# Optimization experiments

Hardware: AMD Instinct MI355X
Metric: run time of the kernel (lower is better)

## Reference

```python
import jax, jax.numpy as jnp
import numpy as np

K = 20
EPS = 1e-5

def get_graph_feature(x, k):
    # x: [B, C, N] -> edge features [B, 2C, N, k]
    xt = jnp.swapaxes(x, 1, 2)  # [B, N, C]
    sq = jnp.sum(xt * xt, axis=-1)  # [B, N]
    # negative squared distance: -(|a|^2 + |b|^2 - 2 a.b)
    pair = 2.0 * jnp.einsum('bnc,bmc->bnm', xt, xt) - sq[:, :, None] - sq[:, None, :]
    idx = jax.lax.top_k(pair, k)[1]  # [B, N, k] nearest neighbors (incl. self)
    neigh = jax.vmap(lambda f, i: f[i])(xt, idx)  # [B, N, k, C]
    ctr = xt[:, :, None, :]  # [B, N, 1, C]
    edge = jnp.concatenate([neigh - ctr, jnp.broadcast_to(ctr, neigh.shape)], axis=-1)  # [B,N,k,2C]
    return jnp.transpose(edge, (0, 3, 1, 2))  # [B, 2C, N, k]

def bn_lrelu(y, g, b, axes):
    # training-mode batchnorm (biased batch stats) + LeakyReLU(0.2)
    m = jnp.mean(y, axis=axes, keepdims=True)
    v = jnp.var(y, axis=axes, keepdims=True)
    shape = [1, -1] + [1] * (y.ndim - 2)
    yn = (y - m) / jnp.sqrt(v + EPS) * g.reshape(shape) + b.reshape(shape)
    return jnp.where(yn >= 0, yn, 0.2 * yn)

def edge_block(x, w, g, b, k):
    e = get_graph_feature(x, k)           # [B, 2C, N, k]
    y = jnp.einsum('bcnk,oc->bonk', e, w)  # 1x1 conv2d, no bias
    y = bn_lrelu(y, g, b, (0, 2, 3))
    return jnp.max(y, axis=-1)            # max over k -> [B, O, N]

def setup_inputs() -> dict:
    key = jax.random.key(0)
    ks = jax.random.split(key, 8)
    B, N = 8, 1024
    num_features = 256
    def w(k_, o, i):
        return jax.random.normal(k_, (o, i), dtype=jnp.float32) * (1.0 / np.sqrt(i))
    d = {
        'x': jax.random.normal(ks[0], (B, N, 3), dtype=jnp.float32),
        'w1': w(ks[1], 64, 6),   'g1': jnp.ones(64),  'b1': jnp.zeros(64),
        'w2': w(ks[2], 64, 128), 'g2': jnp.ones(64),  'b2': jnp.zeros(64),
        'w3': w(ks[3], 128, 128),'g3': jnp.ones(128), 'b3': jnp.zeros(128),
        'w4': w(ks[4], 256, 256),'g4': jnp.ones(256), 'b4': jnp.zeros(256),
        'w5': w(ks[5], 512, 512),'g5': jnp.ones(512), 'b5': jnp.zeros(512),
        'wemb': w(ks[6], num_features, 512),
    }
    return d

def reference(x, w1, g1, b1, w2, g2, b2, w3, g3, b3, w4, g4, b4, w5, g5, b5, wemb):
    xc = jnp.swapaxes(x, 2, 1)  # [B, 3, N]
    x1 = edge_block(xc, w1, g1, b1, K)  # [B, 64, N]
    x2 = edge_block(x1, w2, g2, b2, K)  # [B, 64, N]
    x3 = edge_block(x2, w3, g3, b3, K)  # [B, 128, N]
    x4 = edge_block(x3, w4, g4, b4, K)  # [B, 256, N]
    cat = jnp.concatenate([x1, x2, x3, x4], axis=1)  # [B, 512, N]
    y = jnp.einsum('bcn,oc->bon', cat, w5)            # 1x1 conv1d
    y = bn_lrelu(y, g5, b5, (0, 2))
    feat = jnp.max(y, axis=-1)  # [B, 512]
    return feat @ wemb.T        # [B, num_features]
```

## Files before the change

kernel.cpp:

```cpp
#include <hip/hip_runtime.h>
#include <hip/hip_bf16.h>
#include <math.h>

#define BB 8
#define NN 1024
#define KNNK 20
#define LDC 512

typedef __attribute__((ext_vector_type(8))) short bfrag8;
typedef __attribute__((ext_vector_type(4))) float facc4;
typedef __attribute__((ext_vector_type(2))) float v2f;

struct bh8 { __hip_bfloat16 h[8]; };

__device__ __forceinline__ bh8 cvt8(float4 a, float4 b) {
    bh8 v;
    v.h[0] = __float2bfloat16(a.x); v.h[1] = __float2bfloat16(a.y);
    v.h[2] = __float2bfloat16(a.z); v.h[3] = __float2bfloat16(a.w);
    v.h[4] = __float2bfloat16(b.x); v.h[5] = __float2bfloat16(b.y);
    v.h[6] = __float2bfloat16(b.z); v.h[7] = __float2bfloat16(b.w);
    return v;
}

template<int CTRL, int RMASK>
__device__ __forceinline__ float fmax_dpp(float x) {
    int xi = __float_as_int(x);
    int yi = __builtin_amdgcn_update_dpp(xi, xi, CTRL, RMASK, 0xF, false);
    return fmaxf(x, __int_as_float(yi));
}

__device__ __forceinline__ float wave_max64(float x) {
    x = fmax_dpp<0x121, 0xF>(x);
    x = fmax_dpp<0x122, 0xF>(x);
    x = fmax_dpp<0x124, 0xF>(x);
    x = fmax_dpp<0x128, 0xF>(x);
    x = fmax_dpp<0x142, 0xA>(x);
    x = fmax_dpp<0x143, 0xC>(x);
    return __int_as_float(__builtin_amdgcn_readlane(__float_as_int(x), 63));
}

__device__ __forceinline__ void select20_pf(float (*dist)[1024],
                                            int q0, int w, int lane,
                                            int* __restrict__ idxout) {
    float d[2][16];
    int   sl[2][16];
#pragma unroll
    for (int qi = 0; qi < 2; qi++) {
        int row = w * 2 + qi;
#pragma unroll
        for (int j = 0; j < 16; j++) { d[qi][j] = dist[row][lane + 64 * j]; sl[qi][j] = j; }
    }
    constexpr unsigned char CA[63] = {
        0,2,4,6,8,10,12,14,
        0,1,4,5,8,9,12,13,
        1,5,9,13,
        0,1,2,3,8,9,10,11,
        2,3,10,11,
        1,3,5,9,11,13,
        0,1,2,3,4,5,6,7,
        4,5,6,7,
        2,3,6,7,10,11,
        1,3,5,7,9,11,13};
    constexpr unsigned char CB[63] = {
        1,3,5,7,9,11,13,15,
        2,3,6,7,10,11,14,15,
        2,6,10,14,
        4,5,6,7,12,13,14,15,
        4,5,12,13,
        2,4,6,10,12,14,
        8,9,10,11,12,13,14,15,
        8,9,10,11,
        4,5,8,9,12,13,
        2,4,6,8,10,12,14};
#pragma unroll
    for (int c = 0; c < 63; c++) {
        const int a = CA[c], bq = CB[c];
#pragma unroll
        for (int qi = 0; qi < 2; qi++) {
            bool sw = d[qi][a] < d[qi][bq];
            float dmx = sw ? d[qi][bq] : d[qi][a];
            float dmn = sw ? d[qi][a]  : d[qi][bq];
            d[qi][a] = dmx; d[qi][bq] = dmn;
            int smx = sw ? sl[qi][bq] : sl[qi][a];
            int smn = sw ? sl[qi][a]  : sl[qi][bq];
            sl[qi][a] = smx; sl[qi][bq] = smn;
        }
    }
    unsigned long long slp[2];
#pragma unroll
    for (int qi = 0; qi < 2; qi++) {
        int row = w * 2 + qi;
#pragma unroll
        for (int j = 0; j < 16; j++) dist[row][j * 64 + lane] = d[qi][j];
        unsigned long long p = 0;
#pragma unroll
        for (int j = 0; j < 16; j++) p |= (unsigned long long)sl[qi][j] << (4 * j);
        slp[qi] = p;
    }
    float head[2] = {d[0][0], d[1][0]};
    float pf[2]   = {d[0][1], d[1][1]};
    int   ptr[2]  = {2, 2};
    for (int t = 0; t < KNNK; t++) {
#pragma unroll
        for (int qi = 0; qi < 2; qi++) {
            int row = w * 2 + qi;
            float bv = wave_max64(head[qi]);
            unsigned long long ball = __ballot(head[qi] == bv);
            int wl = (int)__builtin_ctzll(ball);
            bool win = (lane == wl);
            if (win) {
                idxout[(q0 + row) * KNNK + t] = (int)(slp[qi] & 15ull) * 64 + lane;
            }
            head[qi] = win ? pf[qi] : head[qi];
            slp[qi]  = win ? (slp[qi] >> 4) : slp[qi];
            if (win) {
                int p = ptr[qi];
                pf[qi] = (p < 16) ? dist[row][p * 64 + lane] : -INFINITY;
                ptr[qi] = p + 1;
            }
        }
    }
}

__device__ __forceinline__ void zero_r1(float* r1s, float* r1q, int O, int tid) {
    for (int i = tid; i < 32 * O; i += 256) { r1s[i] = 0.f; r1q[i] = 0.f; }
}

__global__ __launch_bounds__(256, 4) void knn3_fused(const float* __restrict__ x,
                                                     const float* __restrict__ w1,
                                                     float* __restrict__ zf,
                                                     int* __restrict__ idxout,
                                                     float* __restrict__ r1s, float* __restrict__ r1q) {
    __shared__ float dist[8][1024];
    int tid = threadIdx.x;
    int q0 = (blockIdx.x & 7) * 1024 + (blockIdx.x >> 3) * 8;
    int b = q0 >> 10;
    if (blockIdx.x == 0) zero_r1(r1s, r1q, 64, tid);
    const float* xb = x + (size_t)b * NN * 3;
    int lane = tid & 63, w = tid >> 6;
    float qx[8], qy[8], qz[8];
#pragma unroll
    for (int q = 0; q < 8; q++) {
        const float* qr = xb + (size_t)((q0 & (NN - 1)) + q) * 3;
        qx[q] = qr[0]; qy[q] = qr[1]; qz[q] = qr[2];
    }
#pragma unroll
    for (int cq = 0; cq < 4; cq++) {
        int cand = w * 256 + cq * 64 + lane;
        const float* cr = xb + (size_t)cand * 3;
        float cx = cr[0], cy = cr[1], cz = cr[2];
        float sqc = 0.f;
        sqc += cx * cx; sqc += cy * cy; sqc += cz * cz;
#pragma unroll
        for (int q = 0; q < 8; q++) {
            float d = qx[q] * cx + qy[q] * cy + qz[q] * cz;
            dist[q][cand] = 2.f * d - sqc;
        }
    }
    for (int i = tid; i < 8 * 128; i += 256) {
        int lq = i >> 7, j = i & 127;
        const float* wr = w1 + (j < 64 ? j * 6 : (j - 64) * 6 + 3);
        const float* xr = x + (size_t)(q0 + lq) * 3;
        zf[(size_t)(q0 + lq) * 128 + j] = wr[0] * xr[0] + wr[1] * xr[1] + wr[2] * xr[2];
    }
    __syncthreads();
    select20_pf(dist, q0, w, lane, idxout);
}

template<int C>
__device__ __forceinline__ void knn_body(const float* __restrict__ xT,
                                         const float* __restrict__ sqn,
                                         int* __restrict__ idxout,
                                         float (*dist)[1024], int knnBlk) {
    int tid = threadIdx.x;
    int q0 = (knnBlk & 7) * 1024 + (knnBlk >> 3) * 8;
    int b = q0 >> 10;
    int lane = tid & 63, w = tid >> 6;
    int cand0 = w * 256 + 4 * lane;
    const float* xTb = xT + (size_t)b * C * 1024;
    const float* qrow = xTb + (q0 & (NN - 1));
    float4 sq4 = *(const float4*)(sqn + b * NN + cand0);
    v2f acc2[4][4];
#pragma unroll
    for (int j = 0; j < 4; j++)
#pragma unroll
        for (int p = 0; p < 4; p++) acc2[j][p] = (v2f){0.f, 0.f};
    for (int cg = 0; cg < C / 4; cg++) {
        float4 rch[4];
#pragma unroll
        for (int c = 0; c < 4; c++)
            rch[c] = *(const float4*)(xTb + (size_t)(4 * cg + c) * 1024 + cand0);
#pragma unroll
        for (int c = 0; c < 4; c++) {
            const float* qr = qrow + (size_t)(4 * cg + c) * 1024;
            float4 qa = *(const float4*)qr;
            float4 qb = *(const float4*)(qr + 4);
            v2f qp[4] = {{qa.x, qa.y}, {qa.z, qa.w}, {qb.x, qb.y}, {qb.z, qb.w}};
            float rj[4] = {rch[c].x, rch[c].y, rch[c].z, rch[c].w};
#pragma unroll
            for (int j = 0; j < 4; j++) {
                v2f rr = {rj[j], rj[j]};
                acc2[j][0] += rr * qp[0];
                acc2[j][1] += rr * qp[1];
                acc2[j][2] += rr * qp[2];
                acc2[j][3] += rr * qp[3];
            }
        }
    }
#pragma unroll
    for (int p = 0; p < 4; p++)
#pragma unroll
        for (int half = 0; half < 2; half++) {
            int q = 2 * p + half;
            float4 dv;
            dv.x = 2.f * acc2[0][p][half] - sq4.x;
            dv.y = 2.f * acc2[1][p][half] - sq4.y;
            dv.z = 2.f * acc2[2][p][half] - sq4.z;
            dv.w = 2.f * acc2[3][p][half] - sq4.w;
            *(float4*)&dist[q][cand0] = dv;
        }
    __syncthreads();
    select20_pf(dist, q0, w, lane, idxout);
}

template<int C, int ZO2>
__global__ __launch_bounds__(256, 4) void knnz_fat(const float* __restrict__ xT,
                                                   const float* __restrict__ xt, int off,
                                                   const float* __restrict__ sqn,
                                                   int* __restrict__ idxout,
                                                   const float* __restrict__ w,
                                                   float* __restrict__ zf,
                                                   float* __restrict__ r1s, float* __restrict__ r1q,
                                                   int Onext) {
    __shared__ float dist[8][1024];
    int tid = threadIdx.x;
    if ((int)blockIdx.x < BB * NN / 8) {
        knn_body<C>(xT, sqn, idxout, dist, blockIdx.x);
        return;
    }
    constexpr int ZO = ZO2 / 2;
    int zblk = blockIdx.x - BB * NN / 8;
    if (zblk == 0) zero_r1(r1s, r1q, Onext, tid);
    float (*xs)[C] = (float (*)[C])&dist[0][0];
    int p0 = zblk * 16;
    for (int j = tid; j < 16 * (C / 4); j += 256) {
        int p = j / (C / 4), c4 = j % (C / 4);
        *(float4*)&xs[p][4 * c4] = *(const float4*)(xt + (size_t)(p0 + p) * LDC + off + 4 * c4);
    }
    __syncthreads();
    for (int j = tid; j < ZO2; j += 256) {
        const float* wr = w + (j < ZO ? (size_t)j * 2 * C : (size_t)(j - ZO) * 2 * C + C);
        float acc[16];
#pragma unroll
        for (int p = 0; p < 16; p++) acc[p] = 0.f;
        for (int c4 = 0; c4 < C / 4; c4++) {
            float4 wv = *(const float4*)(wr + 4 * c4);
#pragma unroll
            for (int p = 0; p < 16; p++) {
                float4 xv = *(const float4*)&xs[p][4 * c4];
                acc[p] += wv.x * xv.x + wv.y * xv.y + wv.z * xv.z + wv.w * xv.w;
            }
        }
#pragma unroll
        for (int p = 0; p < 16; p++) zf[(size_t)(p0 + p) * ZO2 + j] = acc[p];
    }
}

__global__ __launch_bounds__(256, 4) void knnz4_fat(const float* __restrict__ xT,
                                                    const float* __restrict__ sqn,
                                                    int* __restrict__ idxout,
                                                    const float* __restrict__ xtcat,
                                                    const float* __restrict__ w4,
                                                    __hip_bfloat16* __restrict__ zf4,
                                                    float* __restrict__ r1s, float* __restrict__ r1q) {
    __shared__ __align__(16) char smem[36864];
    int tid = threadIdx.x;
    if ((int)blockIdx.x < BB * NN / 8) {
        float (*dist)[1024] = (float (*)[1024])smem;
        if (blockIdx.x == 0) zero_r1(r1s, r1q, 256, tid);
        knn_body<128>(xT, sqn, idxout, dist, blockIdx.x);
        return;
    }
    __hip_bfloat16 (*A)[72] = (__hip_bfloat16 (*)[72])smem;
    __hip_bfloat16 (*W)[72] = (__hip_bfloat16 (*)[72])(smem + 18432);
    int zblk = blockIdx.x - BB * NN / 8;
    int mt = zblk >> 2, nt = zblk & 3;
    int lane = tid & 63, wvx = tid >> 6;
    int mw = wvx >> 1, nw = wvx & 1;
    int m0 = lane & 15, qd = lane >> 4;
    int r = tid & 127, hf = tid >> 7;
    facc4 acc[4][4];
    facc4 zz = {0.f, 0.f, 0.f, 0.f};
#pragma unroll
    for (int mi = 0; mi < 4; mi++)
#pragma unroll
        for (int ni = 0; ni < 4; ni++) acc[mi][ni] = zz;
    int j = nt * 128 + r;
    const float* wsrc = w4 + (j < 256 ? (size_t)j * 256 : (size_t)(j - 256) * 256 + 128);
    const float* asrc = xtcat + (size_t)(mt * 128 + r) * 512 + 128;
    for (int kc = 0; kc < 2; kc++) {
#pragma unroll
        for (int u = 0; u < 4; u++) {
            int c0 = kc * 64 + hf * 32 + 8 * u;
            float4 a0 = *(const float4*)(asrc + c0);
            float4 a1 = *(const float4*)(asrc + c0 + 4);
            *(bh8*)&A[r][hf * 32 + 8 * u] = cvt8(a0, a1);
            float4 w0 = *(const float4*)(wsrc + c0);
            float4 w1 = *(const float4*)(wsrc + c0 + 4);
            *(bh8*)&W[r][hf * 32 + 8 * u] = cvt8(w0, w1);
        }
        __syncthreads();
#pragma unroll
        for (int kk = 0; kk < 2; kk++) {
            bfrag8 af[4], bf[4];
#pragma unroll
            for (int mi = 0; mi < 4; mi++)
                af[mi] = *(const bfrag8*)&A[64 * mw + 16 * mi + m0][32 * kk + 8 * qd];
#pragma unroll
            for (int ni = 0; ni < 4; ni++)
                bf[ni] = *(const bfrag8*)&W[64 * nw + 16 * ni + m0][32 * kk + 8 * qd];
#pragma unroll
            for (int mi = 0; mi < 4; mi++)
#pragma unroll
                for (int ni = 0; ni < 4; ni++)
                    acc[mi][ni] = __builtin_amdgcn_mfma_f32_16x16x32_bf16(af[mi], bf[ni], acc[mi][ni], 0, 0, 0);
        }
        __syncthreads();
    }
#pragma unroll
    for (int mi = 0; mi < 4; mi++)
#pragma unroll
        for (int ni = 0; ni < 4; ni++)
#pragma unroll
            for (int rg = 0; rg < 4; rg++) {
                int row = mt * 128 + mw * 64 + mi * 16 + qd * 4 + rg;
                int col = nt * 128 + nw * 64 + ni * 16 + m0;
                zf4[(size_t)row * 512 + col] = __float2bfloat16(acc[mi][ni][rg]);
            }
}

template<int O2>
__global__ __launch_bounds__(256) void gatherstats_k(const float* __restrict__ zf,
                                                     const int* __restrict__ idx,
                                                     float* __restrict__ ymax, float* __restrict__ ymin,
                                                     float* __restrict__ r1s, float* __restrict__ r1q) {
    constexpr int O = O2 / 2;
    __shared__ float red_s[4][O], red_q[4][O];
    int wv = threadIdx.x >> 6, lane = threadIdx.x & 63;
    int n = (blockIdx.x & 7) * 1024 + (blockIdx.x >> 3) * 4 + wv;
    int b = n >> 10;
    const float* zbatch = zf + (size_t)b * NN * O2;
    int nb[KNNK];
#pragma unroll
    for (int k = 0; k < KNNK; k++) nb[k] = idx[n * KNNK + k];
#pragma unroll
    for (int ch = 0; ch < O / 64; ch++) {
        int o = ch * 64 + lane;
        float g[KNNK];
#pragma unroll
        for (int k = 0; k < KNNK; k++) g[k] = zbatch[(size_t)nb[k] * O2 + o];
        float mx = -INFINITY, mn = INFINITY, s = 0.f, ss = 0.f;
#pragma unroll
        for (int k = 0; k < KNNK; k++) {
            float v = g[k];
            mx = fmaxf(mx, v); mn = fminf(mn, v); s += v; ss += v * v;
        }
        float zn  = zf[(size_t)n * O2 + o];
        float zbn = zf[(size_t)n * O2 + O + o];
        float d = zbn - zn;
        mx += d; mn += d;
        ss = ss + 2.f * d * s + (float)KNNK * d * d;
        s  = s + (float)KNNK * d;
        ymax[(size_t)n * O + o] = mx;
        ymin[(size_t)n * O + o] = mn;
        red_s[wv][o] = s;
        red_q[wv][o] = ss;
    }
    __syncthreads();
    int bucket = blockIdx.x & 31;
    for (int o = threadIdx.x; o < O; o += 256) {
        float s4 = red_s[0][o] + red_s[1][o] + red_s[2][o] + red_s[3][o];
        float q4 = red_q[0][o] + red_q[1][o] + red_q[2][o] + red_q[3][o];
        atomicAdd(&r1s[(size_t)bucket * O + o], s4);
        atomicAdd(&r1q[(size_t)bucket * O + o], q4);
    }
}

__global__ __launch_bounds__(256) void gatherstats4_k(const __hip_bfloat16* __restrict__ zf4,
                                                      const int* __restrict__ idx,
                                                      float* __restrict__ ymax, float* __restrict__ ymin,
                                                      float* __restrict__ r1s, float* __restrict__ r1q) {
    __shared__ float red_s[4][256], red_q[4][256];
    int wv = threadIdx.x >> 6, lane = threadIdx.x & 63;
    int n = (blockIdx.x & 7) * 1024 + (blockIdx.x >> 3) * 4 + wv;
    int b = n >> 10;
    const __hip_bfloat16* zbatch = zf4 + (size_t)b * NN * 512;
    int nb[KNNK];
#pragma unroll
    for (int k = 0; k < KNNK; k++) nb[k] = idx[n * KNNK + k];
#pragma unroll
    for (int ch = 0; ch < 4; ch++) {
        int o = ch * 64 + lane;
        float g[KNNK];
#pragma unroll
        for (int k = 0; k < KNNK; k++) g[k] = __bfloat162float(zbatch[(size_t)nb[k] * 512 + o]);
        float mx = -INFINITY, mn = INFINITY, s = 0.f, ss = 0.f;
#pragma unroll
        for (int k = 0; k < KNNK; k++) {
            float v = g[k];
            mx = fmaxf(mx, v); mn = fminf(mn, v); s += v; ss += v * v;
        }
        float zn  = __bfloat162float(zf4[(size_t)n * 512 + o]);
        float zbn = __bfloat162float(zf4[(size_t)n * 512 + 256 + o]);
        float d = zbn - zn;
        mx += d; mn += d;
        ss = ss + 2.f * d * s + (float)KNNK * d * d;
        s  = s + (float)KNNK * d;
        ymax[(size_t)n * 256 + o] = mx;
        ymin[(size_t)n * 256 + o] = mn;
        red_s[wv][o] = s;
        red_q[wv][o] = ss;
    }
    __syncthreads();
    int bucket = blockIdx.x & 31;
    for (int o = threadIdx.x; o < 256; o += 256) {
        float s4 = red_s[0][o] + red_s[1][o] + red_s[2][o] + red_s[3][o];
        float q4 = red_q[0][o] + red_q[1][o] + red_q[2][o] + red_q[3][o];
        atomicAdd(&r1s[(size_t)bucket * 256 + o], s4);
        atomicAdd(&r1q[(size_t)bucket * 256 + o], q4);
    }
}

template<int O>
__global__ __launch_bounds__(256) void epitrans2_k(const float* __restrict__ ymax, const float* __restrict__ ymin,
                                                   const float* __restrict__ r1s, const float* __restrict__ r1q,
                                                   const float* __restrict__ g, const float* __restrict__ beta,
                                                   double invM,
                                                   float* __restrict__ xtcat, int off_out,
                                                   float* __restrict__ xT, float* __restrict__ sqn,
                                                   __hip_bfloat16* __restrict__ xbf) {
    __shared__ float tile[64][O + 1];
    __shared__ float ssh[O], tth[O];
    int n0 = blockIdx.x * 64;
    int b = n0 >> 10;
    int tid = threadIdx.x;
    for (int o = tid; o < O; o += 256) {
        double sd = 0.0, qd = 0.0;
        for (int r = 0; r < 32; r++) { sd += r1s[(size_t)r * O + o]; qd += r1q[(size_t)r * O + o]; }
        double mean = sd * invM;
        double var = qd * invM - mean * mean;
        float inv = (float)(1.0 / sqrt(var + 1e-5));
        float sc = g[o] * inv;
        ssh[o] = sc;
        tth[o] = beta[o] - (float)mean * sc;
    }
    __syncthreads();
    for (int i = tid; i < 64 * O; i += 256) {
        int nl = i / O;
        int o = i & (O - 1);
        int n = n0 + nl;
        float sc = ssh[o];
        float v = sc >= 0.f ? ymax[(size_t)n * O + o] : ymin[(size_t)n * O + o];
        float y = sc * v + tth[o];
        y = y >= 0.f ? y : 0.2f * y;
        xtcat[(size_t)n * LDC + off_out + o] = y;
        xbf[(size_t)n * LDC + off_out + o] = __float2bfloat16(y);
        tile[nl][o] = y;
    }
    __syncthreads();
    if (tid < 64) {
        float sq = 0.f;
        for (int c = 0; c < O; c++) { float v = tile[tid][c]; sq += v * v; }
        sqn[n0 + tid] = sq;
    }
    int r = tid >> 4, cq = tid & 15;
#pragma unroll
    for (int ct = 0; ct < O / 16; ct++) {
        int c = ct * 16 + r;
        float4 ov;
        ov.x = tile[4 * cq + 0][c];
        ov.y = tile[4 * cq + 1][c];
        ov.z = tile[4 * cq + 2][c];
        ov.w = tile[4 * cq + 3][c];
        *(float4*)(xT + ((size_t)b * O + c) * 1024 + (n0 & (NN - 1)) + 4 * cq) = ov;
    }
}

__global__ __launch_bounds__(256) void epilogue4_k(const float* __restrict__ ymax, const float* __restrict__ ymin,
                                                   const float* __restrict__ r1s, const float* __restrict__ r1q,
                                                   const float* __restrict__ g, const float* __restrict__ beta,
                                                   double invM,
                                                   __hip_bfloat16* __restrict__ xbf) {
    __shared__ float ssh[256], tth[256];
    int n0 = blockIdx.x * 64;
    int tid = threadIdx.x;
    {
        int o = tid;
        double sd = 0.0, qd = 0.0;
        for (int r = 0; r < 32; r++) { sd += r1s[(size_t)r * 256 + o]; qd += r1q[(size_t)r * 256 + o]; }
        double mean = sd * invM;
        double var = qd * invM - mean * mean;
        float inv = (float)(1.0 / sqrt(var + 1e-5));
        float sc = g[o] * inv;
        ssh[o] = sc;
        tth[o] = beta[o] - (float)mean * sc;
    }
    __syncthreads();
    for (int i = tid; i < 64 * 256; i += 256) {
        int nl = i >> 8;
        int o = i & 255;
        int n = n0 + nl;
        float sc = ssh[o];
        float v = sc >= 0.f ? ymax[(size_t)n * 256 + o] : ymin[(size_t)n * 256 + o];
        float y = sc * v + tth[o];
        y = y >= 0.f ? y : 0.2f * y;
        xbf[(size_t)n * LDC + 256 + o] = __float2bfloat16(y);
    }
}

__global__ __launch_bounds__(256) void gemm5_mfma(const __hip_bfloat16* __restrict__ xbf,
                                                  const float* __restrict__ w5,
                                                  float* __restrict__ pmax, float* __restrict__ pmn,
                                                  float* __restrict__ ps, float* __restrict__ pq) {
    __shared__ __hip_bfloat16 A[128][72];
    __shared__ __hip_bfloat16 W[128][72];
    int mt = blockIdx.x >> 2, nt = blockIdx.x & 3;
    int tid = threadIdx.x;
    int lane = tid & 63, wvx = tid >> 6;
    int mw = wvx >> 1, nw = wvx & 1;
    int m0 = lane & 15, qd = lane >> 4;
    int r = tid & 127, hf = tid >> 7;
    facc4 acc[4][4];
    facc4 zz = {0.f, 0.f, 0.f, 0.f};
#pragma unroll
    for (int mi = 0; mi < 4; mi++)
#pragma unroll
        for (int ni = 0; ni < 4; ni++) acc[mi][ni] = zz;
    for (int kc = 0; kc < 8; kc++) {
        const __hip_bfloat16* ap = xbf + (size_t)(mt * 128 + r) * 512 + kc * 64 + hf * 32;
        const float* wp = w5 + (size_t)(nt * 128 + r) * 512 + kc * 64 + hf * 32;
#pragma unroll
        for (int u = 0; u < 4; u++) {
            bh8 av = *(const bh8*)(ap + 8 * u);
            *(bh8*)&A[r][hf * 32 + 8 * u] = av;
            float4 w0 = *(const float4*)(wp + 8 * u);
            float4 w1 = *(const float4*)(wp + 8 * u + 4);
            *(bh8*)&W[r][hf * 32 + 8 * u] = cvt8(w0, w1);
        }
        __syncthreads();
#pragma unroll
        for (int kk = 0; kk < 2; kk++) {
            bfrag8 af[4], bf[4];
#pragma unroll
            for (int mi = 0; mi < 4; mi++)
                af[mi] = *(const bfrag8*)&A[64 * mw + 16 * mi + m0][32 * kk + 8 * qd];
#pragma unroll
            for (int ni = 0; ni < 4; ni++)
                bf[ni] = *(const bfrag8*)&W[64 * nw + 16 * ni + m0][32 * kk + 8 * qd];
#pragma unroll
            for (int mi = 0; mi < 4; mi++)
#pragma unroll
                for (int ni = 0; ni < 4; ni++)
                    acc[mi][ni] = __builtin_amdgcn_mfma_f32_16x16x32_bf16(af[mi], bf[ni], acc[mi][ni], 0, 0, 0);
        }
        __syncthreads();
    }
#pragma unroll
    for (int mi = 0; mi < 4; mi++) {
        int grp = mt * 8 + mw * 4 + mi;
#pragma unroll
        for (int ni = 0; ni < 4; ni++) {
            float mx = -INFINITY, mn = INFINITY, s = 0.f, ss = 0.f;
#pragma unroll
            for (int rg = 0; rg < 4; rg++) {
                float v = acc[mi][ni][rg];
                mx = fmaxf(mx, v); mn = fminf(mn, v); s += v; ss += v * v;
            }
#pragma unroll
            for (int m = 16; m < 64; m <<= 1) {
                mx = fmaxf(mx, __shfl_xor(mx, m));
                mn = fminf(mn, __shfl_xor(mn, m));
                s += __shfl_xor(s, m);
                ss += __shfl_xor(ss, m);
            }
            if (qd == 0) {
                int o = nt * 128 + nw * 64 + ni * 16 + m0;
                pmax[(size_t)grp * 512 + o] = mx;
                pmn [(size_t)grp * 512 + o] = mn;
                ps  [(size_t)grp * 512 + o] = s;
                pq  [(size_t)grp * 512 + o] = ss;
            }
        }
    }
}

__global__ __launch_bounds__(256) void bnstat5_k(const float* __restrict__ ps, const float* __restrict__ pq,
                                                 const float* __restrict__ g, const float* __restrict__ beta,
                                                 float* __restrict__ s_out, float* __restrict__ t_out) {
    __shared__ double lds_s[4][8], lds_q[4][8];
    int tid = threadIdx.x;
    int lane = tid & 63, wv = tid >> 6;
    int ol = lane & 7;
    int rg = wv * 8 + (lane >> 3);
    int o = blockIdx.x * 8 + ol;
    double s = 0.0, q = 0.0;
    for (int r = rg; r < 512; r += 32) {
        s += ps[(size_t)r * 512 + o];
        q += pq[(size_t)r * 512 + o];
    }
    s += __shfl_xor(s, 8);  q += __shfl_xor(q, 8);
    s += __shfl_xor(s, 16); q += __shfl_xor(q, 16);
    s += __shfl_xor(s, 32); q += __shfl_xor(q, 32);
    if (lane < 8) { lds_s[wv][ol] = s; lds_q[wv][ol] = q; }
    __syncthreads();
    if (tid < 8) {
        s = lds_s[0][tid] + lds_s[1][tid] + lds_s[2][tid] + lds_s[3][tid];
        q = lds_q[0][tid] + lds_q[1][tid] + lds_q[2][tid] + lds_q[3][tid];
        double invM = 1.0 / (BB * NN);
        double mean = s * invM;
        double var = q * invM - mean * mean;
        float inv = (float)(1.0 / sqrt(var + 1e-5));
        int oo = blockIdx.x * 8 + tid;
        float sc = g[oo] * inv;
        s_out[oo] = sc;
        t_out[oo] = beta[oo] - (float)mean * sc;
    }
}

__global__ __launch_bounds__(256) void featreduce_k(const float* __restrict__ pmax, const float* __restrict__ pmn,
                                                    const float* __restrict__ s, const float* __restrict__ t,
                                                    float* __restrict__ feat8) {
    __shared__ float smx[4][64], smn[4][64];
    int blk = blockIdx.x;
    int b = blk >> 3, oc = blk & 7;
    int tid = threadIdx.x;
    int lane = tid & 63, wv = tid >> 6;
    int o = oc * 64 + lane;
    float mx = -INFINITY, mn = INFINITY;
    for (int r = b * 64 + wv; r < (b + 1) * 64; r += 4) {
        mx = fmaxf(mx, pmax[(size_t)r * 512 + o]);
        mn = fminf(mn, pmn [(size_t)r * 512 + o]);
    }
    smx[wv][lane] = mx; smn[wv][lane] = mn;
    __syncthreads();
    if (wv == 0) {
        mx = fmaxf(fmaxf(smx[0][lane], smx[1][lane]), fmaxf(smx[2][lane], smx[3][lane]));
        mn = fminf(fminf(smn[0][lane], smn[1][lane]), fminf(smn[2][lane], smn[3][lane]));
        float sc = s[o];
        float v = sc >= 0.f ? mx : mn;
        float y = sc * v + t[o];
        feat8[(size_t)b * 512 + o] = y >= 0.f ? y : 0.2f * y;
    }
}

__global__ __launch_bounds__(256) void outgemm_k(const float* __restrict__ feat8,
                                                 const float* __restrict__ wemb,
                                                 float* __restrict__ out) {
    __shared__ __align__(16) float feat[512];
    int blk = blockIdx.x;
    int b = blk >> 3, nc = blk & 7;
    int tid = threadIdx.x;
    for (int i = tid; i < 512; i += 256) feat[i] = feat8[(size_t)b * 512 + i];
    __syncthreads();
    int o_l = tid >> 3, kc = tid & 7;
    int o = nc * 32 + o_l;
    const float4* wr = (const float4*)(wemb + (size_t)o * 512 + kc * 64);
    const float4* fv = (const float4*)(feat + kc * 64);
    float acc = 0.f;
#pragma unroll
    for (int i = 0; i < 16; i++) {
        float4 wv = wr[i];
        float4 f  = fv[i];
        acc += wv.x * f.x + wv.y * f.y + wv.z * f.z + wv.w * f.w;
    }
    acc += __shfl_xor(acc, 1);
    acc += __shfl_xor(acc, 2);
    acc += __shfl_xor(acc, 4);
    if (kc == 0) out[(size_t)b * 256 + o] = acc;
}

extern "C" void kernel_launch(void* const* d_in, const int* in_sizes, int n_in,
                              void* d_out, int out_size, void* d_ws, size_t ws_size,
                              hipStream_t stream) {
    const float* x    = (const float*)d_in[0];
    const float* w1   = (const float*)d_in[1];
    const float* g1   = (const float*)d_in[2];
    const float* b1   = (const float*)d_in[3];
    const float* w2   = (const float*)d_in[4];
    const float* g2   = (const float*)d_in[5];
    const float* b2   = (const float*)d_in[6];
    const float* w3   = (const float*)d_in[7];
    const float* g3   = (const float*)d_in[8];
    const float* b3   = (const float*)d_in[9];
    const float* w4   = (const float*)d_in[10];
    const float* g4   = (const float*)d_in[11];
    const float* b4   = (const float*)d_in[12];
    const float* w5   = (const float*)d_in[13];
    const float* g5   = (const float*)d_in[14];
    const float* b5   = (const float*)d_in[15];
    const float* wemb = (const float*)d_in[16];
    float* out = (float*)d_out;

    float* fws    = (float*)d_ws;
    float* xtcat  = fws;
    float* ymax   = xtcat + (size_t)BB * NN * 512;
    float* ymin   = ymax + (size_t)BB * NN * 256;
    float* psum   = ymin + (size_t)BB * NN * 256;
    float* psumsq = psum + (size_t)BB * NN * 256;
    float* xT     = psum;
    float* pmax   = ymax;
    float* pmn    = pmax + 512 * 512;
    float* ps5    = pmn + 512 * 512;
    float* pq5    = ps5 + 512 * 512;
    float* feat8  = psumsq;
    float* sqn    = psumsq + (size_t)BB * NN * 256;
    float* s_arr  = sqn + BB * NN;
    float* t_arr  = s_arr + 512;
    float* r1s    = t_arr + 512;
    float* r1q    = r1s + 32 * 512;
    int*   idxb   = (int*)(r1q + 32 * 512);
    float* zfull  = (float*)(idxb + BB * NN * KNNK);
    __hip_bfloat16* zf4 = (__hip_bfloat16*)zfull;
    __hip_bfloat16* xbf = (__hip_bfloat16*)(zfull + (size_t)BB * NN * 512);

    const double invM_edge = 1.0 / ((double)BB * NN * KNNK);
    const int nbn = BB * NN;
    const int NK = nbn / 8;
    const int NZ = nbn / 16;

    knn3_fused<<<NK, 256, 0, stream>>>(x, w1, zfull, idxb, r1s, r1q);
    gatherstats_k<128><<<nbn / 4, 256, 0, stream>>>(zfull, idxb, ymax, ymin, r1s, r1q);
    epitrans2_k<64><<<128, 256, 0, stream>>>(ymax, ymin, r1s, r1q, g1, b1, invM_edge, xtcat, 0, xT, sqn, xbf);

    knnz_fat<64, 128><<<NK + NZ, 256, 0, stream>>>(xT, xtcat, 0, sqn, idxb, w2, zfull, r1s, r1q, 64);
    gatherstats_k<128><<<nbn / 4, 256, 0, stream>>>(zfull, idxb, ymax, ymin, r1s, r1q);
    epitrans2_k<64><<<128, 256, 0, stream>>>(ymax, ymin, r1s, r1q, g2, b2, invM_edge, xtcat, 64, xT, sqn, xbf);

    knnz_fat<64, 256><<<NK + NZ, 256, 0, stream>>>(xT, xtcat, 64, sqn, idxb, w3, zfull, r1s, r1q, 128);
    gatherstats_k<256><<<nbn / 4, 256, 0, stream>>>(zfull, idxb, ymax, ymin, r1s, r1q);
    epitrans2_k<128><<<128, 256, 0, stream>>>(ymax, ymin, r1s, r1q, g3, b3, invM_edge, xtcat, 128, xT, sqn, xbf);

    knnz4_fat<<<NK + 256, 256, 0, stream>>>(xT, sqn, idxb, xtcat, w4, zf4, r1s, r1q);
    gatherstats4_k<<<nbn / 4, 256, 0, stream>>>(zf4, idxb, ymax, ymin, r1s, r1q);
    epilogue4_k<<<128, 256, 0, stream>>>(ymax, ymin, r1s, r1q, g4, b4, invM_edge, xbf);

    gemm5_mfma<<<256, 256, 0, stream>>>(xbf, w5, pmax, pmn, ps5, pq5);
    bnstat5_k<<<64, 256, 0, stream>>>(ps5, pq5, g5, b5, s_arr, t_arr);
    featreduce_k<<<64, 256, 0, stream>>>(pmax, pmn, s_arr, t_arr, feat8);
    outgemm_k<<<64, 256, 0, stream>>>(feat8, wemb, out);
}
```

Baseline: 330.7 us.

## Raise occupancy hints, reorder fused block roles, shrink GEMM LDS tiles, split epilogue

The fused kNN/projection kernels get a higher min-blocks-per-SM launch bound. The fused kernels now put the GEMM blocks first in the grid and the kNN blocks after them, so the short projection work starts early. The layer-4 MFMA tile loop now stages K in 32-wide chunks, which shrinks LDS from 36 KB to 32 KB but doubles the number of barriers. The layer-4 epilogue uses twice as many blocks, each covering half the points, at the cost of repeating the BN stat reduction per block. A tighter register budget could cause spills.

Measured after the change: 351.6 us. 1.06x slower.

```diff
diff --git a/kernel.cpp b/kernel.cpp
--- a/kernel.cpp
+++ b/kernel.cpp
@@ -126,7 +126,7 @@
     for (int i = tid; i < 32 * O; i += 256) { r1s[i] = 0.f; r1q[i] = 0.f; }
 }
 
-__global__ __launch_bounds__(256, 4) void knn3_fused(const float* __restrict__ x,
+__global__ __launch_bounds__(256, 5) void knn3_fused(const float* __restrict__ x,
                                                      const float* __restrict__ w1,
                                                      float* __restrict__ zf,
                                                      int* __restrict__ idxout,
@@ -224,7 +224,7 @@
 }
 
 template<int C, int ZO2>
-__global__ __launch_bounds__(256, 4) void knnz_fat(const float* __restrict__ xT,
+__global__ __launch_bounds__(256, 5) void knnz_fat(const float* __restrict__ xT,
                                                    const float* __restrict__ xt, int off,
                                                    const float* __restrict__ sqn,
                                                    int* __restrict__ idxout,
@@ -234,12 +234,12 @@
                                                    int Onext) {
     __shared__ float dist[8][1024];
     int tid = threadIdx.x;
-    if ((int)blockIdx.x < BB * NN / 8) {
-        knn_body<C>(xT, sqn, idxout, dist, blockIdx.x);
+    if ((int)blockIdx.x >= BB * NN / 16) {
+        knn_body<C>(xT, sqn, idxout, dist, blockIdx.x - BB * NN / 16);
         return;
     }
     constexpr int ZO = ZO2 / 2;
-    int zblk = blockIdx.x - BB * NN / 8;
+    int zblk = blockIdx.x;
     if (zblk == 0) zero_r1(r1s, r1q, Onext, tid);
     float (*xs)[C] = (float (*)[C])&dist[0][0];
     int p0 = zblk * 16;
@@ -266,24 +266,24 @@
     }
 }
 
-__global__ __launch_bounds__(256, 4) void knnz4_fat(const float* __restrict__ xT,
+__global__ __launch_bounds__(256, 5) void knnz4_fat(const float* __restrict__ xT,
                                                     const float* __restrict__ sqn,
                                                     int* __restrict__ idxout,
                                                     const float* __restrict__ xtcat,
                                                     const float* __restrict__ w4,
                                                     __hip_bfloat16* __restrict__ zf4,
                                                     float* __restrict__ r1s, float* __restrict__ r1q) {
-    __shared__ __align__(16) char smem[36864];
-    int tid = threadIdx.x;
-    if ((int)blockIdx.x < BB * NN / 8) {
+    __shared__ __align__(16) char smem[32768];
+    int tid = threadIdx.x;
+    if ((int)blockIdx.x >= 256) {
         float (*dist)[1024] = (float (*)[1024])smem;
-        if (blockIdx.x == 0) zero_r1(r1s, r1q, 256, tid);
-        knn_body<128>(xT, sqn, idxout, dist, blockIdx.x);
+        knn_body<128>(xT, sqn, idxout, dist, blockIdx.x - 256);
         return;
     }
-    __hip_bfloat16 (*A)[72] = (__hip_bfloat16 (*)[72])smem;
-    __hip_bfloat16 (*W)[72] = (__hip_bfloat16 (*)[72])(smem + 18432);
-    int zblk = blockIdx.x - BB * NN / 8;
+    __hip_bfloat16 (*A)[40] = (__hip_bfloat16 (*)[40])smem;
+    __hip_bfloat16 (*W)[40] = (__hip_bfloat16 (*)[40])(smem + 10240);
+    if (blockIdx.x == 0) zero_r1(r1s, r1q, 256, tid);
+    int zblk = blockIdx.x;
     int mt = zblk >> 2, nt = zblk & 3;
     int lane = tid & 63, wvx = tid >> 6;
     int mw = wvx >> 1, nw = wvx & 1;
@@ -298,33 +298,34 @@
     int j = nt * 128 + r;
     const float* wsrc = w4 + (j < 256 ? (size_t)j * 256 : (size_t)(j - 256) * 256 + 128);
     const float* asrc = xtcat + (size_t)(mt * 128 + r) * 512 + 128;
-    for (int kc = 0; kc < 2; kc++) {
-#pragma unroll
-        for (int u = 0; u < 4; u++) {
-            int c0 = kc * 64 + hf * 32 + 8 * u;
-            float4 a0 = *(const float4*)(asrc + c0);
-            float4 a1 = *(const float4*)(asrc + c0 + 4);
-            *(bh8*)&A[r][hf * 32 + 8 * u] = cvt8(a0, a1);
-            float4 w0 = *(const float4*)(wsrc + c0);
-            float4 w1 = *(const float4*)(wsrc + c0 + 4);
-            *(bh8*)&W[r][hf * 32 + 8 * u] = cvt8(w0, w1);
-        }
+#pragma unroll
+    for (int kc = 0; kc < 4; kc++) {
+        int c0 = kc * 32 + hf * 16;
+        float4 a0 = *(const float4*)(asrc + c0);
+        float4 a1 = *(const float4*)(asrc + c0 + 4);
+        float4 a2 = *(const float4*)(asrc + c0 + 8);
+        float4 a3 = *(const float4*)(asrc + c0 + 12);
+        *(bh8*)&A[r][hf * 16]     = cvt8(a0, a1);
+        *(bh8*)&A[r][hf * 16 + 8] = cvt8(a2, a3);
+        float4 w0 = *(const float4*)(wsrc + c0);
+        float4 w1 = *(const float4*)(wsrc + c0 + 4);
+        float4 w2 = *(const float4*)(wsrc + c0 + 8);
+        float4 w3 = *(const float4*)(wsrc + c0 + 12);
+        *(bh8*)&W[r][hf * 16]     = cvt8(w0, w1);
+        *(bh8*)&W[r][hf * 16 + 8] = cvt8(w2, w3);
         __syncthreads();
-#pragma unroll
-        for (int kk = 0; kk < 2; kk++) {
-            bfrag8 af[4], bf[4];
-#pragma unroll
-            for (int mi = 0; mi < 4; mi++)
-                af[mi] = *(const bfrag8*)&A[64 * mw + 16 * mi + m0][32 * kk + 8 * qd];
+        bfrag8 af[4], bf[4];
+#pragma unroll
+        for (int mi = 0; mi < 4; mi++)
+            af[mi] = *(const bfrag8*)&A[64 * mw + 16 * mi + m0][8 * qd];
+#pragma unroll
+        for (int ni = 0; ni < 4; ni++)
+            bf[ni] = *(const bfrag8*)&W[64 * nw + 16 * ni + m0][8 * qd];
+#pragma unroll
+        for (int mi = 0; mi < 4; mi++)
 #pragma unroll
             for (int ni = 0; ni < 4; ni++)
-                bf[ni] = *(const bfrag8*)&W[64 * nw + 16 * ni + m0][32 * kk + 8 * qd];
-#pragma unroll
-            for (int mi = 0; mi < 4; mi++)
-#pragma unroll
-                for (int ni = 0; ni < 4; ni++)
-                    acc[mi][ni] = __builtin_amdgcn_mfma_f32_16x16x32_bf16(af[mi], bf[ni], acc[mi][ni], 0, 0, 0);
-        }
+                acc[mi][ni] = __builtin_amdgcn_mfma_f32_16x16x32_bf16(af[mi], bf[ni], acc[mi][ni], 0, 0, 0);
         __syncthreads();
     }
 #pragma unroll
@@ -492,7 +493,7 @@
                                                    double invM,
                                                    __hip_bfloat16* __restrict__ xbf) {
     __shared__ float ssh[256], tth[256];
-    int n0 = blockIdx.x * 64;
+    int n0 = blockIdx.x * 32;
     int tid = threadIdx.x;
     {
         int o = tid;
@@ -506,7 +507,7 @@
         tth[o] = beta[o] - (float)mean * sc;
     }
     __syncthreads();
-    for (int i = tid; i < 64 * 256; i += 256) {
+    for (int i = tid; i < 32 * 256; i += 256) {
         int nl = i >> 8;
         int o = i & 255;
         int n = n0 + nl;
@@ -742,7 +743,7 @@
 
     knnz4_fat<<<NK + 256, 256, 0, stream>>>(xT, sqn, idxb, xtcat, w4, zf4, r1s, r1q);
     gatherstats4_k<<<nbn / 4, 256, 0, stream>>>(zf4, idxb, ymax, ymin, r1s, r1q);
-    epilogue4_k<<<128, 256, 0, stream>>>(ymax, ymin, r1s, r1q, g4, b4, invM_edge, xbf);
+    epilogue4_k<<<256, 256, 0, stream>>>(ymax, ymin, r1s, r1q, g4, b4, invM_edge, xbf);
 
     gemm5_mfma<<<256, 256, 0, stream>>>(xbf, w5, pmax, pmn, ps5, pq5);
     bnstat5_k<<<64, 256, 0, stream>>>(ps5, pq5, g5, b5, s_arr, t_arr);
```
